# Performance work log

Measured on AMD Instinct MI355X. Metric: run time of the kernel, lower is better.

## Reference

```python
import jax, jax.numpy as jnp
import numpy as np
from jax import lax

B, N, H, D = 4, 384, 8, 5          # graphs, nodes/graph, heads, max multi-hop dist
NE, E_TOT, DH, L = 2048, 8192, 256, 10  # edges/graph, total real edges, d_hidden, curve samples
N_SPATIAL, N_EDGE_DIST = 64, 128


def _bn(x, g, b):
    # eval-mode BatchNorm1d (running_mean=0, running_var=1): affine only
    return x * g + b


def _conv1d(x, w):
    # x: [E, C, L], w: [O, I, 3], SAME padding, stride 1
    return lax.conv_general_dilated(x, w, (1,), 'SAME',
                                    dimension_numbers=('NCH', 'OIH', 'NCH'))


def setup_inputs() -> dict:
    key = jax.random.key(0)
    ks = iter(jax.random.split(key, 64))
    nrm = lambda shape, s=0.02: jax.random.normal(next(ks), shape, jnp.float32) * s
    std = 0.02 / np.sqrt(12.0)  # init_params with n_layer=12 for Linear weights
    inp = {}
    inp['attn_bias'] = jax.random.normal(next(ks), (B, N + 1, N + 1), jnp.float32)
    inp['spatial_pos'] = jax.random.randint(next(ks), (B, N, N), 0, N_SPATIAL)
    inp['d2_dist'] = jax.random.normal(next(ks), (B, N, N, 32), jnp.float32)
    inp['a3_dist'] = jax.random.normal(next(ks), (B, N, N, 32), jnp.float32)
    inp['edge_data'] = jax.random.normal(next(ks), (E_TOT, L, 7), jnp.float32)
    inp['edge_path'] = jax.random.randint(next(ks), (B, N, N, D), 0, NE + 1)
    inp['edge_padding_mask'] = jnp.zeros((B, NE), bool)  # all real edges
    inp['src'] = jax.random.randint(next(ks), (E_TOT,), 0, B * N)
    inp['dst'] = jax.random.randint(next(ks), (E_TOT,), 0, B * N)
    inp['node_data'] = jax.random.normal(next(ks), (B * N, DH), jnp.float32)
    # --- parameters ---
    inp['spatial_emb'] = nrm((N_SPATIAL, H)).at[0].set(0.0)  # padding_idx=0
    inp['t_virtual'] = nrm((1, H))
    inp['w_d2'] = nrm((H, 32), std); inp['b_d2'] = jnp.zeros((H,), jnp.float32)
    inp['w_a3'] = nrm((H, 32), std); inp['b_a3'] = jnp.zeros((H,), jnp.float32)
    inp['cw1'] = nrm((64, 7, 3), std);  inp['cg1'] = jnp.ones((64,));  inp['cb1'] = jnp.zeros((64,))
    inp['cw2'] = nrm((128, 64, 3), std); inp['cg2'] = jnp.ones((128,)); inp['cb2'] = jnp.zeros((128,))
    inp['cw3'] = nrm((256, 128, 3), std); inp['cg3'] = jnp.ones((256,)); inp['cb3'] = jnp.zeros((256,))
    inp['cw_out'] = nrm((H, 256), std)
    # _EdgeConv (UV-Net style): proj Linear(d_hidden->H), MLP(H->64->H), BN, GIN eps
    inp['wp'] = nrm((H, DH), std); inp['bp'] = jnp.zeros((H,))
    inp['w1'] = nrm((64, H), std); inp['b1'] = jnp.zeros((64,))
    inp['g1'] = jnp.ones((64,)); inp['bb1'] = jnp.zeros((64,))
    inp['w2'] = nrm((H, 64), std); inp['b2'] = jnp.zeros((H,))
    inp['g_out'] = jnp.ones((H,)); inp['bb_out'] = jnp.zeros((H,))
    inp['eps'] = jnp.zeros((), jnp.float32)
    inp['edge_dis_w'] = nrm((N_EDGE_DIST * H * H, 1))
    return inp


def reference(attn_bias, spatial_pos, d2_dist, a3_dist, edge_data, edge_path,
              edge_padding_mask, src, dst, node_data, spatial_emb, t_virtual,
              w_d2, b_d2, w_a3, b_a3, cw1, cg1, cb1, cw2, cg2, cb2, cw3, cg3, cb3,
              cw_out, wp, bp, w1, b1, g1, bb1, w2, b2, g_out, bb_out, eps, edge_dis_w):
    gab = jnp.repeat(attn_bias[:, None], H, axis=1)            # [B,H,N+1,N+1]
    spb = spatial_emb[spatial_pos]                              # [B,N,N,H]
    d2b = d2_dist @ w_d2.T + b_d2                               # [B,N,N,H]
    a3b = a3_dist @ w_a3.T + b_a3                               # [B,N,N,H]
    # CurveEncoder on per-edge curve samples
    x = jnp.transpose(edge_data, (0, 2, 1))                     # [E,7,L]
    x = jax.nn.leaky_relu(_bn(_conv1d(x, cw1), cg1[:, None], cb1[:, None]))
    x = jax.nn.leaky_relu(_bn(_conv1d(x, cw2), cg2[:, None], cb2[:, None]))
    x = jax.nn.leaky_relu(_bn(_conv1d(x, cw3), cg3[:, None], cb3[:, None]))
    ef = jnp.mean(x, axis=-1) @ cw_out.T                        # [E,H]
    # _EdgeConv: combine endpoint node features with edge features
    proj = node_data @ wp.T + bp                                # [B*N,H]
    h = (1.0 + eps) * ef + proj[src] + proj[dst]
    h = jax.nn.relu(_bn(h @ w1.T + b1, g1, bb1)) @ w2.T + b2
    edge_out = jax.nn.relu(_bn(h, g_out, bb_out))               # [E,H]
    # scatter real-edge features into padded table (row NE stays zero = padding)
    valid = (~edge_padding_mask).reshape(-1)                    # [B*NE]
    gidx = jnp.maximum(jnp.cumsum(valid) - 1, 0)
    vals = jnp.where(valid[:, None], edge_out[gidx], 0.0).reshape(B, NE, H)
    edge_feature = jnp.zeros((B, NE + 1, H), edge_out.dtype).at[:, :NE].set(vals)
    # gather along multi-hop paths, per-distance head mixing (bmm), normalize
    ep = edge_path.reshape(B, N * N * D)
    edge_input = jax.vmap(lambda f, p: f[p])(edge_feature, ep)  # [B,N*N*D,H]
    edge_input = edge_input.reshape(B, N, N, D, H)
    wdis = edge_dis_w.reshape(-1, H, H)[:D]                     # [D,H,H]
    edge_input = jnp.einsum('bijdh,dhk->bijdk', edge_input, wdis)
    sp = jnp.where(spatial_pos == 0, 1, spatial_pos)
    sp = jnp.where(sp > 1, sp - 1, sp)
    sp = jnp.clip(sp, 0, D)
    edge_bias = edge_input.sum(-2) / sp[..., None].astype(edge_input.dtype)
    inner = spb + d2b + a3b + edge_bias                         # [B,N,N,H]
    gab = gab.at[:, :, 1:, 1:].add(jnp.transpose(inner, (0, 3, 1, 2)))
    t = t_virtual.reshape(1, H, 1)
    gab = gab.at[:, :, 1:, 0].add(t)
    gab = gab.at[:, :, 0, :].add(t)
    return gab + attn_bias[:, None]
```

## Files before the change

kernel.cpp:

```cpp
#include <hip/hip_runtime.h>

#define NB    4
#define NNODE 384
#define NH    8
#define ND    5
#define NEDGE 2048
#define NEP1  2049
#define ETOT  8192
#define DHID  256
#define NP1   385
#define SQ1   (NP1*NP1)
#define NPOS  98304
#define NPOS2 (NPOS + 2)
#define NCELL (NB*NNODE*NNODE)

typedef __attribute__((ext_vector_type(8)))  short short8;
typedef __attribute__((ext_vector_type(16))) float float16;

__device__ __forceinline__ unsigned short f2bf(float f) {
    union { float f; unsigned int u; } v; v.f = f;
    unsigned int u = v.u;
    return (unsigned short)((u + 0x7FFFu + ((u >> 16) & 1u)) >> 16);
}
__device__ __forceinline__ float bf2f(unsigned short s) {
    union { unsigned int u; float f; } v; v.u = ((unsigned int)s) << 16; return v.f;
}
__device__ __forceinline__ unsigned pkbf(float a, float b) {
    return (unsigned)f2bf(a) | ((unsigned)f2bf(b) << 16);
}
__device__ __forceinline__ short8 mk8(unsigned a, unsigned b, unsigned c, unsigned d) {
    union { unsigned u[4]; short8 s; } x; x.u[0]=a; x.u[1]=b; x.u[2]=c; x.u[3]=d; return x.s;
}
__device__ __forceinline__ float leaky(float v) { return v > 0.f ? v : 0.01f * v; }
__device__ __forceinline__ float16 zero16() {
    float16 z;
#pragma unroll
    for (int i = 0; i < 16; ++i) z[i] = 0.f;
    return z;
}
__device__ __forceinline__ void gl_lds16(const void* g, void* l) {
    __builtin_amdgcn_global_load_lds(
        (const __attribute__((address_space(1))) unsigned int*)g,
        (__attribute__((address_space(3))) unsigned int*)l,
        16, 0, 0);
}

__global__ __launch_bounds__(256) void prep_kernel(
    const float* __restrict__ cw1, const float* __restrict__ cw2, const float* __restrict__ cw3,
    const float* __restrict__ cw_out,
    const float* __restrict__ node_data, const float* __restrict__ wp, const float* __restrict__ bp,
    unsigned short* __restrict__ W1f, unsigned short* __restrict__ W2f, unsigned short* __restrict__ W3f,
    unsigned short* __restrict__ Wof,
    float* __restrict__ proj, float* __restrict__ edge_feature)
{
    int gid = blockIdx.x * 256 + threadIdx.x;
    if (gid < 98304) {
        int j = gid & 7, lane = (gid >> 3) & 63, blk = gid >> 9;
        int ks = blk & 7, tp = (blk >> 3) % 3, mt = blk / 24;
        int oc = mt * 32 + (lane & 31);
        int ic = ks * 16 + (lane >> 5) * 8 + j;
        W3f[gid] = f2bf(cw3[(oc * 128 + ic) * 3 + tp]);
    } else if (gid < 122880) {
        int f = gid - 98304;
        int j = f & 7, lane = (f >> 3) & 63, blk = f >> 9;
        int ks = blk & 3, tp = (blk >> 2) % 3, mt = blk / 12;
        int oc = mt * 32 + (lane & 31);
        int ic = ks * 16 + (lane >> 5) * 8 + j;
        W2f[f] = f2bf(cw2[(oc * 64 + ic) * 3 + tp]);
    } else if (gid < 124928) {
        int f = gid - 122880;
        int j = f & 7, lane = (f >> 3) & 63, blk = f >> 9;
        int ks = blk & 1, mt = blk >> 1;
        int oc = mt * 32 + (lane & 31);
        int k = ks * 16 + (lane >> 5) * 8 + j;
        int tp = k >> 3, c = k & 7;
        float v = (tp < 3 && c < 7) ? cw1[oc * 21 + c * 3 + tp] : 0.f;
        W1f[f] = f2bf(v);
    } else if (gid < 137216) {
        int f = gid - 124928;
        int v = f >> 3, h = f & 7;
        const float4* nd4 = (const float4*)(node_data + (size_t)v * DHID);
        const float4* ww4 = (const float4*)(wp + (size_t)h * DHID);
        float s0 = 0.f, s1 = 0.f, s2 = 0.f, s3 = 0.f;
#pragma unroll 4
        for (int c = 0; c < 64; c += 4) {
            float4 x0 = nd4[c+0], y0 = ww4[c+0];
            float4 x1 = nd4[c+1], y1 = ww4[c+1];
            float4 x2 = nd4[c+2], y2 = ww4[c+2];
            float4 x3 = nd4[c+3], y3 = ww4[c+3];
            s0 += x0.x*y0.x + x0.y*y0.y + x0.z*y0.z + x0.w*y0.w;
            s1 += x1.x*y1.x + x1.y*y1.y + x1.z*y1.z + x1.w*y1.w;
            s2 += x2.x*y2.x + x2.y*y2.y + x2.z*y2.z + x2.w*y2.w;
            s3 += x3.x*y3.x + x3.y*y3.y + x3.z*y3.z + x3.w*y3.w;
        }
        proj[f] = bp[h] + (s0 + s1) + (s2 + s3);
    } else if (gid < 137248) {
        int f = gid - 137216;
        int b = f >> 3, h = f & 7;
        edge_feature[((size_t)b * NEP1 + NEDGE) * NH + h] = 0.f;
    } else if (gid < 145440) {
        int f = gid - 137248;
        int j = f & 7, lane = (f >> 3) & 63, g = f >> 9;
        int m = lane & 31;
        int k = g * 16 + (lane >> 5) * 8 + j;
        Wof[f] = (m < 8) ? f2bf(cw_out[m * 256 + k]) : (unsigned short)0;
    }
}

#define X0_GROWS 8
__global__ __launch_bounds__(256) void pack_kernel(
    const float* __restrict__ edge_data,
    unsigned short* __restrict__ X0buf, unsigned short* __restrict__ X1buf,
    unsigned short* __restrict__ X2buf)
{
    int gid = blockIdx.x * 256 + threadIdx.x;
    const int NX0 = (NPOS + 2 * X0_GROWS) * 8;
    if (gid < NX0) {
        int row = gid >> 3, ch = gid & 7;
        int pos = row - X0_GROWS;
        unsigned short v = 0;
        if (pos >= 0 && pos < NPOS && ch < 7) {
            int pm = pos % 12;
            if (pm >= 1 && pm <= 10)
                v = f2bf(edge_data[(size_t)(pos / 12) * 70 + (pm - 1) * 7 + ch]);
        }
        X0buf[gid] = v;
    } else if (gid < NX0 + 128) {
        int f = gid - NX0;
        int p = f >> 5, rest = f & 31;
        int row = (rest >> 4) ? (NPOS + 1) : 0, col = rest & 15;
        X1buf[((size_t)p * NPOS2 + row) * 16 + col] = 0;
    } else if (gid < NX0 + 128 + 256) {
        int f = gid - NX0 - 128;
        int p = f >> 5, rest = f & 31;
        int row = (rest >> 4) ? (NPOS + 1) : 0, col = rest & 15;
        X2buf[((size_t)p * NPOS2 + row) * 16 + col] = 0;
    }
}

__global__ __launch_bounds__(256, 4) void conv1_kernel(
    const unsigned short* __restrict__ X0, const unsigned short* __restrict__ W1f,
    const float* __restrict__ cg1, const float* __restrict__ cb1,
    unsigned short* __restrict__ X1)
{
    const int t = threadIdx.x, wv = t >> 6, lane = t & 63;
    const int q = lane >> 5, n = lane & 31;
    const int pos = blockIdx.x * 128 + wv * 32 + n;

    float16 acc0 = zero16(), acc1 = zero16();
#pragma unroll
    for (int ks = 0; ks < 2; ++ks) {
        short8 b  = *(const short8*)(X0 + (pos - 1 + 2 * ks + q) * 8);
        short8 a0 = *(const short8*)(W1f + ((0 * 2 + ks) * 64 + lane) * 8);
        short8 a1 = *(const short8*)(W1f + ((1 * 2 + ks) * 64 + lane) * 8);
        acc0 = __builtin_amdgcn_mfma_f32_32x32x16_bf16(a0, b, acc0, 0, 0, 0);
        acc1 = __builtin_amdgcn_mfma_f32_32x32x16_bf16(a1, b, acc1, 0, 0, 0);
    }
    int pm = pos % 12;
    bool valid = (pm != 0) && (pm != 11);
#pragma unroll
    for (int mt = 0; mt < 2; ++mt) {
        const float16& acc = mt ? acc1 : acc0;
#pragma unroll
        for (int r2 = 0; r2 < 4; ++r2) {
            int oc0 = mt * 32 + 8 * r2 + 4 * q;
            float4 g4 = *(const float4*)(cg1 + oc0);
            float4 b4 = *(const float4*)(cb1 + oc0);
            unsigned short uu[4];
            uu[0] = valid ? f2bf(leaky(acc[r2*4+0] * g4.x + b4.x)) : (unsigned short)0;
            uu[1] = valid ? f2bf(leaky(acc[r2*4+1] * g4.y + b4.y)) : (unsigned short)0;
            uu[2] = valid ? f2bf(leaky(acc[r2*4+2] * g4.z + b4.z)) : (unsigned short)0;
            uu[3] = valid ? f2bf(leaky(acc[r2*4+3] * g4.w + b4.w)) : (unsigned short)0;
            uint2 pk; pk.x = uu[0] | ((unsigned)uu[1] << 16); pk.y = uu[2] | ((unsigned)uu[3] << 16);
            *(uint2*)(void*)(X1 + ((size_t)(oc0 >> 4) * NPOS2 + pos + 1) * 16 + (oc0 & 15)) = pk;
        }
    }
}

__global__ __launch_bounds__(256, 4) void conv2_kernel(
    const unsigned short* __restrict__ X1, const unsigned short* __restrict__ W2f,
    const float* __restrict__ cg2, const float* __restrict__ cb2,
    unsigned short* __restrict__ X2)
{
    __shared__ __align__(16) unsigned short sB[4][1568];
    const int t = threadIdx.x, wv = t >> 6, lane = t & 63;
    const int q = lane >> 5, n = lane & 31;
    const int base = blockIdx.x * 96;
    const int cbase = (wv < 3) ? wv * 64 : 132;

#pragma unroll
    for (int ks = 0; ks < 4; ++ks)
        gl_lds16(X1 + ((size_t)ks * NPOS2 + base) * 16 + (cbase + lane) * 8,
                 &sB[ks][cbase * 8]);

    float16 acc[3];
#pragma unroll
    for (int nt = 0; nt < 3; ++nt) acc[nt] = zero16();

    __syncthreads();

#pragma unroll
    for (int ks = 0; ks < 4; ++ks)
#pragma unroll
        for (int tp = 0; tp < 3; ++tp) {
            short8 a = *(const short8*)(W2f + (((wv * 3 + tp) * 4 + ks) * 64 + lane) * 8);
#pragma unroll
            for (int nt = 0; nt < 3; ++nt) {
                short8 b = *(const short8*)(&sB[ks][(nt * 32 + n + tp) * 16 + q * 8]);
                acc[nt] = __builtin_amdgcn_mfma_f32_32x32x16_bf16(a, b, acc[nt], 0, 0, 0);
            }
        }

#pragma unroll
    for (int nt = 0; nt < 3; ++nt) {
        int pos = base + nt * 32 + n;
        int pm = pos % 12;
        bool valid = (pm != 0) && (pm != 11);
#pragma unroll
        for (int r2 = 0; r2 < 4; ++r2) {
            int oc0 = wv * 32 + 8 * r2 + 4 * q;
            float4 g4 = *(const float4*)(cg2 + oc0);
            float4 b4 = *(const float4*)(cb2 + oc0);
            unsigned short uu[4];
            uu[0] = valid ? f2bf(leaky(acc[nt][r2*4+0] * g4.x + b4.x)) : (unsigned short)0;
            uu[1] = valid ? f2bf(leaky(acc[nt][r2*4+1] * g4.y + b4.y)) : (unsigned short)0;
            uu[2] = valid ? f2bf(leaky(acc[nt][r2*4+2] * g4.z + b4.z)) : (unsigned short)0;
            uu[3] = valid ? f2bf(leaky(acc[nt][r2*4+3] * g4.w + b4.w)) : (unsigned short)0;
            uint2 pk; pk.x = uu[0] | ((unsigned)uu[1] << 16); pk.y = uu[2] | ((unsigned)uu[3] << 16);
            *(uint2*)(void*)(X2 + ((size_t)(oc0 >> 4) * NPOS2 + pos + 1) * 16 + (oc0 & 15)) = pk;
        }
    }
}

__global__ __launch_bounds__(256, 3) void conv3_kernel(
    const unsigned short* __restrict__ X2, const unsigned short* __restrict__ W3f,
    const unsigned short* __restrict__ Wof,
    const float* __restrict__ cg3, const float* __restrict__ cb3,
    const int* __restrict__ src, const int* __restrict__ dst,
    const float* __restrict__ w1, const float* __restrict__ b1,
    const float* __restrict__ g1, const float* __restrict__ bb1,
    const float* __restrict__ w2, const float* __restrict__ b2,
    const float* __restrict__ g_out, const float* __restrict__ bb_out,
    const float* __restrict__ eps, const float* __restrict__ proj,
    float* __restrict__ edge_feature)
{
    __shared__ __align__(16) unsigned char smem3[25088];
    unsigned short* sB = (unsigned short*)smem3;
    float* fs = (float*)smem3;
    const int t = threadIdx.x, wv = t >> 6, lane = t & 63;
    const int q = lane >> 5, n = lane & 31;
    const int base = blockIdx.x * 96;
    const int cbase = (wv < 3) ? wv * 64 : 132;

#pragma unroll
    for (int ks = 0; ks < 8; ++ks)
        gl_lds16(X2 + ((size_t)ks * NPOS2 + base) * 16 + (cbase + lane) * 8,
                 &sB[ks * 1568 + cbase * 8]);

    float16 acc[2][3];
#pragma unroll
    for (int i = 0; i < 2; ++i)
#pragma unroll
        for (int nt = 0; nt < 3; ++nt) acc[i][nt] = zero16();

    __syncthreads();

#pragma unroll
    for (int ks = 0; ks < 8; ++ks)
#pragma unroll
        for (int tp = 0; tp < 3; ++tp) {
            short8 a0 = *(const short8*)(W3f + ((((wv*2+0) * 3 + tp) * 8 + ks) * 64 + lane) * 8);
            short8 a1 = *(const short8*)(W3f + ((((wv*2+1) * 3 + tp) * 8 + ks) * 64 + lane) * 8);
#pragma unroll
            for (int nt = 0; nt < 3; ++nt) {
                short8 b = *(const short8*)(&sB[ks * 1568 + (nt * 32 + n + tp) * 16 + q * 8]);
                acc[0][nt] = __builtin_amdgcn_mfma_f32_32x32x16_bf16(a0, b, acc[0][nt], 0, 0, 0);
                acc[1][nt] = __builtin_amdgcn_mfma_f32_32x32x16_bf16(a1, b, acc[1][nt], 0, 0, 0);
            }
        }

    __syncthreads();

    short8 wof[4];
#pragma unroll
    for (int g = 0; g < 4; ++g)
        wof[g] = *(const short8*)(Wof + ((wv * 4 + g) * 64 + lane) * 8);

#pragma unroll
    for (int nt = 0; nt < 3; ++nt) {
        int pm = (nt * 32 + n) % 12;
        bool valid = (pm != 0) && (pm != 11);
        float16 p = zero16();
#pragma unroll
        for (int i = 0; i < 2; ++i) {
            int mt = wv * 2 + i;
            float av[16];
#pragma unroll
            for (int r2 = 0; r2 < 4; ++r2) {
                int oc0 = mt * 32 + 8 * r2 + 4 * q;
                float4 g4 = *(const float4*)(cg3 + oc0);
                float4 b4 = *(const float4*)(cb3 + oc0);
                av[r2*4+0] = valid ? leaky(acc[i][nt][r2*4+0] * g4.x + b4.x) : 0.f;
                av[r2*4+1] = valid ? leaky(acc[i][nt][r2*4+1] * g4.y + b4.y) : 0.f;
                av[r2*4+2] = valid ? leaky(acc[i][nt][r2*4+2] * g4.z + b4.z) : 0.f;
                av[r2*4+3] = valid ? leaky(acc[i][nt][r2*4+3] * g4.w + b4.w) : 0.f;
            }
            unsigned pk[8], op[8];
#pragma unroll
            for (int z = 0; z < 8; ++z) pk[z] = pkbf(av[2*z], av[2*z+1]);
#pragma unroll
            for (int z = 0; z < 8; ++z) op[z] = __shfl_xor((int)pk[z], 32);
            short8 f0 = q == 0 ? mk8(pk[0], pk[1], op[0], op[1])
                               : mk8(op[2], op[3], pk[2], pk[3]);
            short8 f1 = q == 0 ? mk8(pk[4], pk[5], op[4], op[5])
                               : mk8(op[6], op[7], pk[6], pk[7]);
            p = __builtin_amdgcn_mfma_f32_32x32x16_bf16(wof[i*2+0], f0, p, 0, 0, 0);
            p = __builtin_amdgcn_mfma_f32_32x32x16_bf16(wof[i*2+1], f1, p, 0, 0, 0);
        }
        float4 st = make_float4(p[0], p[1], p[2], p[3]);
        *(float4*)&fs[((wv * 96) + nt * 32 + n) * 8 + 4 * q] = st;
    }
    __syncthreads();

    if (t < 64) {
        int e = t >> 3, h = t & 7;
        float s = 0.f;
#pragma unroll
        for (int w = 0; w < 4; ++w)
#pragma unroll 4
            for (int l = 0; l < 12; ++l) s += fs[(w * 96 + e * 12 + l) * 8 + h];
        float efv = 0.1f * s;
        int ge = blockIdx.x * 8 + e;
        fs[3072 + e * 8 + h] = (1.f + eps[0]) * efv
                             + proj[src[ge] * NH + h] + proj[dst[ge] * NH + h];
    }
    __syncthreads();

#pragma unroll
    for (int bb = 0; bb < 512; bb += 256) {
        int idx = bb + t;
        int e = idx >> 6, o = idx & 63;
        float a = b1[o];
#pragma unroll
        for (int h = 0; h < 8; ++h) a += fs[3072 + e * 8 + h] * w1[o * 8 + h];
        float v = a * g1[o] + bb1[o];
        fs[3136 + e * 64 + o] = v > 0.f ? v : 0.f;
    }
    __syncthreads();

    if (t < 64) {
        int e = t >> 3, h = t & 7;
        float a = b2[h];
#pragma unroll 8
        for (int o = 0; o < 64; ++o) a += fs[3136 + e * 64 + o] * w2[h * 64 + o];
        float v = a * g_out[h] + bb_out[h];
        v = v > 0.f ? v : 0.f;
        int ge = blockIdx.x * 8 + e;
        int b = ge >> 11, el2 = ge & (NEDGE - 1);
        edge_feature[((size_t)b * NEP1 + el2) * NH + h] = v;
    }
}

__global__ __launch_bounds__(256) void eins_kernel(
    const float* __restrict__ d2_dist, const float* __restrict__ a3_dist,
    const float* __restrict__ w_d2, const float* __restrict__ w_a3,
    unsigned short* __restrict__ acc8)
{
    const int t = threadIdx.x, part = t & 7;
    float4 wd[8], wa[8];
#pragma unroll
    for (int h = 0; h < 8; ++h) {
        wd[h] = *(const float4*)(w_d2 + h * 32 + part * 4);
        wa[h] = *(const float4*)(w_a3 + h * 32 + part * 4);
    }
    const bool pb0 = part & 1, pb1 = (part >> 1) & 1, pb2 = (part >> 2) & 1;
    const size_t stride = 73728;
    size_t cell = (size_t)blockIdx.x * 32 + (t >> 3);

    float4 vd = ((const float4*)(d2_dist + cell * 32))[part];
    float4 va = ((const float4*)(a3_dist + cell * 32))[part];
#pragma unroll 1
    for (int it = 0; it < 8; ++it) {
        float4 nvd = vd, nva = va;
        if (it < 7) {
            nvd = ((const float4*)(d2_dist + (cell + stride) * 32))[part];
            nva = ((const float4*)(a3_dist + (cell + stride) * 32))[part];
        }
        float acc[8];
#pragma unroll
        for (int h = 0; h < 8; ++h)
            acc[h] = vd.x*wd[h].x + vd.y*wd[h].y + vd.z*wd[h].z + vd.w*wd[h].w
                   + va.x*wa[h].x + va.y*wa[h].y + va.z*wa[h].z + va.w*wa[h].w;
        float y0 = (pb0 ? acc[1] : acc[0]) + __shfl_xor(pb0 ? acc[0] : acc[1], 1, 64);
        float y1 = (pb0 ? acc[3] : acc[2]) + __shfl_xor(pb0 ? acc[2] : acc[3], 1, 64);
        float y2 = (pb0 ? acc[5] : acc[4]) + __shfl_xor(pb0 ? acc[4] : acc[5], 1, 64);
        float y3 = (pb0 ? acc[7] : acc[6]) + __shfl_xor(pb0 ? acc[6] : acc[7], 1, 64);
        float z0 = (pb1 ? y1 : y0) + __shfl_xor(pb1 ? y0 : y1, 2, 64);
        float z1 = (pb1 ? y3 : y2) + __shfl_xor(pb1 ? y2 : y3, 2, 64);
        float rr = (pb2 ? z1 : z0) + __shfl_xor(pb2 ? z0 : z1, 4, 64);
        acc8[cell * 8 + part] = f2bf(rr);
        cell += stride;
        vd = nvd; va = nva;
    }
}

__global__ __launch_bounds__(256) void tbl_kernel(
    const float* __restrict__ edge_feature, const float* __restrict__ edge_dis_w,
    float* __restrict__ T)
{
    int idx = blockIdx.x * 256 + threadIdx.x;
    if (idx >= NEP1 * 8) return;
    int pi = idx >> 3, k = idx & 7;
    int d = blockIdx.y, b = blockIdx.z;
    const float* ef = edge_feature + ((size_t)b * NEP1 + pi) * NH;
    const float* w  = edge_dis_w + d * 64 + k;
    float s = 0.f;
#pragma unroll
    for (int h = 0; h < 8; ++h) s += ef[h] * w[h * 8];
    T[(((size_t)b * ND + d) * NEP1 + pi) * 8 + k] = s;
}

__global__ __launch_bounds__(256) void bias_kernel(
    const float* __restrict__ attn_bias, const int* __restrict__ spatial_pos,
    const int* __restrict__ edge_path,
    const float* __restrict__ spatial_emb, const float* __restrict__ t_virtual,
    const float* __restrict__ b_d2, const float* __restrict__ b_a3,
    const float* __restrict__ Tbl, const unsigned short* __restrict__ acc8,
    float* __restrict__ out)
{
    __shared__ __align__(16) float s_emb[512];
    int t = threadIdx.x;
    for (int i = t; i < 512; i += 256) s_emb[i] = spatial_emb[i];
    __syncthreads();

    int gc = blockIdx.x * 256 + t;
    if (gc >= NB * SQ1) return;
    int b = gc / SQ1, rem = gc % SQ1;
    int i = rem / NP1, j = rem % NP1;
    float base = 2.f * attn_bias[gc];
    bool border = (i == 0) || (j == 0);

    float res[8];
    if (border) {
#pragma unroll
        for (int h = 0; h < 8; ++h) res[h] = base + t_virtual[h];
    } else {
        size_t nidx = ((size_t)b * NNODE + (i - 1)) * NNODE + (j - 1);
        int sp = spatial_pos[nidx];
        union { uint4 u; unsigned short s[8]; } aa;
        aa.u = *(const uint4*)(acc8 + nidx * 8);
        const int* ep = edge_path + nidx * ND;
        const float* Tb = Tbl + (size_t)b * (ND * NEP1 * 8);
        float edp[8] = {0,0,0,0,0,0,0,0};
#pragma unroll
        for (int d = 0; d < ND; ++d) {
            const float* r = Tb + ((size_t)d * NEP1 + ep[d]) * 8;
            float4 r0 = *(const float4*)r;
            float4 r1 = *(const float4*)(r + 4);
            edp[0] += r0.x; edp[1] += r0.y; edp[2] += r0.z; edp[3] += r0.w;
            edp[4] += r1.x; edp[5] += r1.y; edp[6] += r1.z; edp[7] += r1.w;
        }
        int spd = (sp == 0) ? 1 : sp;
        spd = (spd > 1) ? spd - 1 : spd;
        spd = (spd > ND) ? ND : spd;
        float inv = 1.f / (float)spd;
        const float* em = s_emb + sp * 8;
#pragma unroll
        for (int h = 0; h < 8; ++h)
            res[h] = base + bf2f(aa.s[h]) + edp[h] * inv + em[h] + b_d2[h] + b_a3[h];
    }
#pragma unroll
    for (int h = 0; h < 8; ++h)
        out[((size_t)b * NH + h) * SQ1 + rem] = res[h];
}

extern "C" void kernel_launch(void* const* d_in, const int* in_sizes, int n_in,
                              void* d_out, int out_size, void* d_ws, size_t ws_size,
                              hipStream_t stream)
{
    const float* attn_bias   = (const float*)d_in[0];
    const int*   spatial_pos = (const int*)  d_in[1];
    const float* d2_dist     = (const float*)d_in[2];
    const float* a3_dist     = (const float*)d_in[3];
    const float* edge_data   = (const float*)d_in[4];
    const int*   edge_path   = (const int*)  d_in[5];
    const int*   src         = (const int*)  d_in[7];
    const int*   dst         = (const int*)  d_in[8];
    const float* node_data   = (const float*)d_in[9];
    const float* spatial_emb = (const float*)d_in[10];
    const float* t_virtual   = (const float*)d_in[11];
    const float* w_d2        = (const float*)d_in[12];
    const float* b_d2        = (const float*)d_in[13];
    const float* w_a3        = (const float*)d_in[14];
    const float* b_a3        = (const float*)d_in[15];
    const float* cw1         = (const float*)d_in[16];
    const float* cg1         = (const float*)d_in[17];
    const float* cb1         = (const float*)d_in[18];
    const float* cw2         = (const float*)d_in[19];
    const float* cg2         = (const float*)d_in[20];
    const float* cb2         = (const float*)d_in[21];
    const float* cw3         = (const float*)d_in[22];
    const float* cg3         = (const float*)d_in[23];
    const float* cb3         = (const float*)d_in[24];
    const float* cw_out      = (const float*)d_in[25];
    const float* wp          = (const float*)d_in[26];
    const float* bp          = (const float*)d_in[27];
    const float* w1          = (const float*)d_in[28];
    const float* b1          = (const float*)d_in[29];
    const float* g1          = (const float*)d_in[30];
    const float* bb1         = (const float*)d_in[31];
    const float* w2          = (const float*)d_in[32];
    const float* b2          = (const float*)d_in[33];
    const float* g_out       = (const float*)d_in[34];
    const float* bb_out      = (const float*)d_in[35];
    const float* eps         = (const float*)d_in[36];
    const float* edge_dis_w  = (const float*)d_in[37];

    float*          proj  = (float*)d_ws;
    float*          ef    = proj + NB * NNODE * NH;
    unsigned short* W1f   = (unsigned short*)(ef + NB * NEP1 * NH);
    unsigned short* W2f   = W1f + 2048;
    unsigned short* W3f   = W2f + 24576;
    unsigned short* Wof   = W3f + 98304;
    unsigned short* X0buf = Wof + 8192;
    unsigned short* X1buf = X0buf + (size_t)(NPOS + 2 * X0_GROWS) * 8;
    unsigned short* X2buf = X1buf + (size_t)4 * NPOS2 * 16;
    unsigned short* X0 = X0buf + X0_GROWS * 8;
    float*          Tbl   = (float*)X0buf;
    unsigned short* acc8  = X1buf;

    prep_kernel<<<569, 256, 0, stream>>>(cw1, cw2, cw3, cw_out, node_data, wp, bp,
                                         W1f, W2f, W3f, Wof, proj, ef);
    pack_kernel<<<3074, 256, 0, stream>>>(edge_data, X0buf, X1buf, X2buf);

    conv1_kernel<<<NPOS / 128, 256, 0, stream>>>(X0, W1f, cg1, cb1, X1buf);
    conv2_kernel<<<NPOS / 96, 256, 0, stream>>>(X1buf, W2f, cg2, cb2, X2buf);

    eins_kernel<<<2304, 256, 0, stream>>>(d2_dist, a3_dist, w_d2, w_a3, acc8);

    conv3_kernel<<<NPOS / 96, 256, 0, stream>>>(X2buf, W3f, Wof, cg3, cb3,
                                                src, dst, w1, b1, g1, bb1,
                                                w2, b2, g_out, bb_out, eps,
                                                proj, ef);

    dim3 tgrid((NEP1 * 8 + 255) / 256, ND, NB);
    tbl_kernel<<<tgrid, 256, 0, stream>>>(ef, edge_dis_w, Tbl);

    int nbias = (NB * SQ1 + 255) / 256;
    bias_kernel<<<nbias, 256, 0, stream>>>(
        attn_bias, spatial_pos, edge_path,
        spatial_emb, t_virtual, b_d2, b_a3,
        Tbl, acc8, (float*)d_out);
}
```

Baseline: 358.7 us.

## Make conv kernels persistent with register-resident weights and double-buffered LDS tiles

conv2 and conv3 now hold their weight fragments and BN scale/shift in registers. Each block loops over several 96-position tiles, prefetching the next tile into a second LDS buffer while the current one is computed. conv3 splits its output channels across a second grid dimension, writes partial projections to a global buffer, and hands the edge MLP to a new edge_tail_kernel. The intent is to cut repeated weight loads and hide global-to-LDS latency, at the cost of more registers, lower occupancy, an extra kernel launch and a global round trip. The eins kernel is moved after conv3 and tbl because Pglob aliases the buffer it writes.

```diff
diff --git a/kernel.cpp b/kernel.cpp
--- a/kernel.cpp
+++ b/kernel.cpp
@@ -177,65 +177,185 @@
     }
 }
 
-__global__ __launch_bounds__(256, 4) void conv2_kernel(
+__global__ __launch_bounds__(256, 2) void conv2_kernel(
     const unsigned short* __restrict__ X1, const unsigned short* __restrict__ W2f,
     const float* __restrict__ cg2, const float* __restrict__ cb2,
     unsigned short* __restrict__ X2)
 {
-    __shared__ __align__(16) unsigned short sB[4][1568];
+    __shared__ __align__(16) unsigned short sB[2][4 * 1568];
     const int t = threadIdx.x, wv = t >> 6, lane = t & 63;
     const int q = lane >> 5, n = lane & 31;
-    const int base = blockIdx.x * 96;
     const int cbase = (wv < 3) ? wv * 64 : 132;
+    const int pbase0 = blockIdx.x * 192;
+
+    short8 a[3][4];
+#pragma unroll
+    for (int tp = 0; tp < 3; ++tp)
+#pragma unroll
+        for (int ks = 0; ks < 4; ++ks)
+            a[tp][ks] = *(const short8*)(W2f + (((wv * 3 + tp) * 4 + ks) * 64 + lane) * 8);
+
+    float4 g4[4], b4[4];
+#pragma unroll
+    for (int r2 = 0; r2 < 4; ++r2) {
+        g4[r2] = *(const float4*)(cg2 + wv * 32 + 8 * r2 + 4 * q);
+        b4[r2] = *(const float4*)(cb2 + wv * 32 + 8 * r2 + 4 * q);
+    }
 
 #pragma unroll
     for (int ks = 0; ks < 4; ++ks)
-        gl_lds16(X1 + ((size_t)ks * NPOS2 + base) * 16 + (cbase + lane) * 8,
-                 &sB[ks][cbase * 8]);
-
-    float16 acc[3];
-#pragma unroll
-    for (int nt = 0; nt < 3; ++nt) acc[nt] = zero16();
-
-    __syncthreads();
-
-#pragma unroll
-    for (int ks = 0; ks < 4; ++ks)
-#pragma unroll
-        for (int tp = 0; tp < 3; ++tp) {
-            short8 a = *(const short8*)(W2f + (((wv * 3 + tp) * 4 + ks) * 64 + lane) * 8);
-#pragma unroll
-            for (int nt = 0; nt < 3; ++nt) {
-                short8 b = *(const short8*)(&sB[ks][(nt * 32 + n + tp) * 16 + q * 8]);
-                acc[nt] = __builtin_amdgcn_mfma_f32_32x32x16_bf16(a, b, acc[nt], 0, 0, 0);
+        gl_lds16(X1 + ((size_t)ks * NPOS2 + pbase0) * 16 + (cbase + lane) * 8,
+                 &sB[0][ks * 1568 + cbase * 8]);
+
+#pragma unroll 1
+    for (int pt = 0; pt < 2; ++pt) {
+        const int cur = pt & 1;
+        const int base = pbase0 + pt * 96;
+        __syncthreads();
+        if (pt < 1) {
+#pragma unroll
+            for (int ks = 0; ks < 4; ++ks)
+                gl_lds16(X1 + ((size_t)ks * NPOS2 + base + 96) * 16 + (cbase + lane) * 8,
+                         &sB[cur ^ 1][ks * 1568 + cbase * 8]);
+        }
+        float16 acc[3];
+#pragma unroll
+        for (int nt = 0; nt < 3; ++nt) acc[nt] = zero16();
+#pragma unroll
+        for (int ks = 0; ks < 4; ++ks)
+#pragma unroll
+            for (int tp = 0; tp < 3; ++tp)
+#pragma unroll
+                for (int nt = 0; nt < 3; ++nt) {
+                    short8 b = *(const short8*)(&sB[cur][ks * 1568 + (nt * 32 + n + tp) * 16 + q * 8]);
+                    acc[nt] = __builtin_amdgcn_mfma_f32_32x32x16_bf16(a[tp][ks], b, acc[nt], 0, 0, 0);
+                }
+#pragma unroll
+        for (int nt = 0; nt < 3; ++nt) {
+            int pos = base + nt * 32 + n;
+            int pm = (nt * 32 + n) % 12;
+            bool valid = (pm != 0) && (pm != 11);
+#pragma unroll
+            for (int r2 = 0; r2 < 4; ++r2) {
+                int oc0 = wv * 32 + 8 * r2 + 4 * q;
+                unsigned short uu[4];
+                uu[0] = valid ? f2bf(leaky(acc[nt][r2*4+0] * g4[r2].x + b4[r2].x)) : (unsigned short)0;
+                uu[1] = valid ? f2bf(leaky(acc[nt][r2*4+1] * g4[r2].y + b4[r2].y)) : (unsigned short)0;
+                uu[2] = valid ? f2bf(leaky(acc[nt][r2*4+2] * g4[r2].z + b4[r2].z)) : (unsigned short)0;
+                uu[3] = valid ? f2bf(leaky(acc[nt][r2*4+3] * g4[r2].w + b4[r2].w)) : (unsigned short)0;
+                uint2 pk; pk.x = uu[0] | ((unsigned)uu[1] << 16); pk.y = uu[2] | ((unsigned)uu[3] << 16);
+                *(uint2*)(void*)(X2 + ((size_t)(oc0 >> 4) * NPOS2 + pos + 1) * 16 + (oc0 & 15)) = pk;
             }
         }
-
-#pragma unroll
-    for (int nt = 0; nt < 3; ++nt) {
-        int pos = base + nt * 32 + n;
-        int pm = pos % 12;
-        bool valid = (pm != 0) && (pm != 11);
-#pragma unroll
-        for (int r2 = 0; r2 < 4; ++r2) {
-            int oc0 = wv * 32 + 8 * r2 + 4 * q;
-            float4 g4 = *(const float4*)(cg2 + oc0);
-            float4 b4 = *(const float4*)(cb2 + oc0);
-            unsigned short uu[4];
-            uu[0] = valid ? f2bf(leaky(acc[nt][r2*4+0] * g4.x + b4.x)) : (unsigned short)0;
-            uu[1] = valid ? f2bf(leaky(acc[nt][r2*4+1] * g4.y + b4.y)) : (unsigned short)0;
-            uu[2] = valid ? f2bf(leaky(acc[nt][r2*4+2] * g4.z + b4.z)) : (unsigned short)0;
-            uu[3] = valid ? f2bf(leaky(acc[nt][r2*4+3] * g4.w + b4.w)) : (unsigned short)0;
-            uint2 pk; pk.x = uu[0] | ((unsigned)uu[1] << 16); pk.y = uu[2] | ((unsigned)uu[3] << 16);
-            *(uint2*)(void*)(X2 + ((size_t)(oc0 >> 4) * NPOS2 + pos + 1) * 16 + (oc0 & 15)) = pk;
-        }
-    }
-}
-
-__global__ __launch_bounds__(256, 3) void conv3_kernel(
+    }
+}
+
+__global__ __launch_bounds__(256, 2) void conv3_kernel(
     const unsigned short* __restrict__ X2, const unsigned short* __restrict__ W3f,
     const unsigned short* __restrict__ Wof,
     const float* __restrict__ cg3, const float* __restrict__ cb3,
+    float* __restrict__ Pglob)
+{
+    __shared__ __align__(16) unsigned short sB[2][8 * 1568];
+    __shared__ float fs[768];
+    const int t = threadIdx.x, wv = t >> 6, lane = t & 63;
+    const int q = lane >> 5, n = lane & 31;
+    const int gy = blockIdx.y;
+    const int mt = gy * 4 + wv;
+    const int cbase = (wv < 3) ? wv * 64 : 132;
+    const int pbase0 = blockIdx.x * 384;
+
+    short8 a[3][8];
+#pragma unroll
+    for (int tp = 0; tp < 3; ++tp)
+#pragma unroll
+        for (int ks = 0; ks < 8; ++ks)
+            a[tp][ks] = *(const short8*)(W3f + (((mt * 3 + tp) * 8 + ks) * 64 + lane) * 8);
+    short8 wof0 = *(const short8*)(Wof + ((2 * mt + 0) * 64 + lane) * 8);
+    short8 wof1 = *(const short8*)(Wof + ((2 * mt + 1) * 64 + lane) * 8);
+
+    float4 g4[4], b4[4];
+#pragma unroll
+    for (int r2 = 0; r2 < 4; ++r2) {
+        g4[r2] = *(const float4*)(cg3 + mt * 32 + 8 * r2 + 4 * q);
+        b4[r2] = *(const float4*)(cb3 + mt * 32 + 8 * r2 + 4 * q);
+    }
+
+#pragma unroll
+    for (int ks = 0; ks < 8; ++ks)
+        gl_lds16(X2 + ((size_t)ks * NPOS2 + pbase0) * 16 + (cbase + lane) * 8,
+                 &sB[0][ks * 1568 + cbase * 8]);
+
+#pragma unroll 1
+    for (int pt = 0; pt < 4; ++pt) {
+        const int cur = pt & 1;
+        const int base = pbase0 + pt * 96;
+        __syncthreads();
+        if (pt < 3) {
+#pragma unroll
+            for (int ks = 0; ks < 8; ++ks)
+                gl_lds16(X2 + ((size_t)ks * NPOS2 + base + 96) * 16 + (cbase + lane) * 8,
+                         &sB[cur ^ 1][ks * 1568 + cbase * 8]);
+        }
+        fs[t] = 0.f; fs[256 + t] = 0.f; fs[512 + t] = 0.f;
+
+        float16 acc[3];
+#pragma unroll
+        for (int nt = 0; nt < 3; ++nt) acc[nt] = zero16();
+#pragma unroll
+        for (int ks = 0; ks < 8; ++ks)
+#pragma unroll
+            for (int tp = 0; tp < 3; ++tp)
+#pragma unroll
+                for (int nt = 0; nt < 3; ++nt) {
+                    short8 b = *(const short8*)(&sB[cur][ks * 1568 + (nt * 32 + n + tp) * 16 + q * 8]);
+                    acc[nt] = __builtin_amdgcn_mfma_f32_32x32x16_bf16(a[tp][ks], b, acc[nt], 0, 0, 0);
+                }
+
+        float4 pout[3];
+#pragma unroll
+        for (int nt = 0; nt < 3; ++nt) {
+            int pm = (nt * 32 + n) % 12;
+            bool valid = (pm != 0) && (pm != 11);
+            float av[16];
+#pragma unroll
+            for (int r2 = 0; r2 < 4; ++r2) {
+                av[r2*4+0] = valid ? leaky(acc[nt][r2*4+0] * g4[r2].x + b4[r2].x) : 0.f;
+                av[r2*4+1] = valid ? leaky(acc[nt][r2*4+1] * g4[r2].y + b4[r2].y) : 0.f;
+                av[r2*4+2] = valid ? leaky(acc[nt][r2*4+2] * g4[r2].z + b4[r2].z) : 0.f;
+                av[r2*4+3] = valid ? leaky(acc[nt][r2*4+3] * g4[r2].w + b4[r2].w) : 0.f;
+            }
+            unsigned pk[8], op[8];
+#pragma unroll
+            for (int z = 0; z < 8; ++z) pk[z] = pkbf(av[2*z], av[2*z+1]);
+#pragma unroll
+            for (int z = 0; z < 8; ++z) op[z] = __shfl_xor((int)pk[z], 32);
+            short8 f0 = q == 0 ? mk8(pk[0], pk[1], op[0], op[1])
+                               : mk8(op[2], op[3], pk[2], pk[3]);
+            short8 f1 = q == 0 ? mk8(pk[4], pk[5], op[4], op[5])
+                               : mk8(op[6], op[7], pk[6], pk[7]);
+            float16 p = zero16();
+            p = __builtin_amdgcn_mfma_f32_32x32x16_bf16(wof0, f0, p, 0, 0, 0);
+            p = __builtin_amdgcn_mfma_f32_32x32x16_bf16(wof1, f1, p, 0, 0, 0);
+            pout[nt] = make_float4(p[0], p[1], p[2], p[3]);
+        }
+        __syncthreads();
+#pragma unroll
+        for (int nt = 0; nt < 3; ++nt) {
+            int o = (nt * 32 + n) * 8 + 4 * q;
+            atomicAdd(&fs[o + 0], pout[nt].x);
+            atomicAdd(&fs[o + 1], pout[nt].y);
+            atomicAdd(&fs[o + 2], pout[nt].z);
+            atomicAdd(&fs[o + 3], pout[nt].w);
+        }
+        __syncthreads();
+        float* Pg = Pglob + ((size_t)gy * NPOS + base) * 8;
+        Pg[t] = fs[t]; Pg[256 + t] = fs[256 + t]; Pg[512 + t] = fs[512 + t];
+    }
+}
+
+__global__ __launch_bounds__(256) void edge_tail_kernel(
+    const float* __restrict__ Pglob,
     const int* __restrict__ src, const int* __restrict__ dst,
     const float* __restrict__ w1, const float* __restrict__ b1,
     const float* __restrict__ g1, const float* __restrict__ bb1,
@@ -244,121 +364,41 @@
     const float* __restrict__ eps, const float* __restrict__ proj,
     float* __restrict__ edge_feature)
 {
-    __shared__ __align__(16) unsigned char smem3[25088];
-    unsigned short* sB = (unsigned short*)smem3;
-    float* fs = (float*)smem3;
-    const int t = threadIdx.x, wv = t >> 6, lane = t & 63;
-    const int q = lane >> 5, n = lane & 31;
-    const int base = blockIdx.x * 96;
-    const int cbase = (wv < 3) ? wv * 64 : 132;
-
-#pragma unroll
-    for (int ks = 0; ks < 8; ++ks)
-        gl_lds16(X2 + ((size_t)ks * NPOS2 + base) * 16 + (cbase + lane) * 8,
-                 &sB[ks * 1568 + cbase * 8]);
-
-    float16 acc[2][3];
-#pragma unroll
-    for (int i = 0; i < 2; ++i)
-#pragma unroll
-        for (int nt = 0; nt < 3; ++nt) acc[i][nt] = zero16();
-
+    __shared__ float s_h[32 * 8];
+    __shared__ float s_t1[32 * 64];
+    const int t = threadIdx.x;
+    const int e = t >> 3, h = t & 7;
+    const int ge = blockIdx.x * 32 + e;
+
+    const float* P0 = Pglob + (size_t)(ge * 12) * 8 + h;
+    const float* P1 = Pglob + ((size_t)NPOS + ge * 12) * 8 + h;
+    float s = 0.f;
+#pragma unroll
+    for (int l = 0; l < 12; ++l) s += P0[l * 8] + P1[l * 8];
+    float efv = 0.1f * s;
+    s_h[e * 8 + h] = (1.f + eps[0]) * efv
+                   + proj[src[ge] * NH + h] + proj[dst[ge] * NH + h];
     __syncthreads();
 
 #pragma unroll
-    for (int ks = 0; ks < 8; ++ks)
-#pragma unroll
-        for (int tp = 0; tp < 3; ++tp) {
-            short8 a0 = *(const short8*)(W3f + ((((wv*2+0) * 3 + tp) * 8 + ks) * 64 + lane) * 8);
-            short8 a1 = *(const short8*)(W3f + ((((wv*2+1) * 3 + tp) * 8 + ks) * 64 + lane) * 8);
-#pragma unroll
-            for (int nt = 0; nt < 3; ++nt) {
-                short8 b = *(const short8*)(&sB[ks * 1568 + (nt * 32 + n + tp) * 16 + q * 8]);
-                acc[0][nt] = __builtin_amdgcn_mfma_f32_32x32x16_bf16(a0, b, acc[0][nt], 0, 0, 0);
-                acc[1][nt] = __builtin_amdgcn_mfma_f32_32x32x16_bf16(a1, b, acc[1][nt], 0, 0, 0);
-            }
-        }
-
+    for (int r = 0; r < 8; ++r) {
+        int idx = r * 256 + t;
+        int ee = idx >> 6, o = idx & 63;
+        float a = b1[o];
+#pragma unroll
+        for (int h2 = 0; h2 < 8; ++h2) a += s_h[ee * 8 + h2] * w1[o * 8 + h2];
+        float v = a * g1[o] + bb1[o];
+        s_t1[ee * 64 + o] = v > 0.f ? v : 0.f;
+    }
     __syncthreads();
 
-    short8 wof[4];
-#pragma unroll
-    for (int g = 0; g < 4; ++g)
-        wof[g] = *(const short8*)(Wof + ((wv * 4 + g) * 64 + lane) * 8);
-
-#pragma unroll
-    for (int nt = 0; nt < 3; ++nt) {
-        int pm = (nt * 32 + n) % 12;
-        bool valid = (pm != 0) && (pm != 11);
-        float16 p = zero16();
-#pragma unroll
-        for (int i = 0; i < 2; ++i) {
-            int mt = wv * 2 + i;
-            float av[16];
-#pragma unroll
-            for (int r2 = 0; r2 < 4; ++r2) {
-                int oc0 = mt * 32 + 8 * r2 + 4 * q;
-                float4 g4 = *(const float4*)(cg3 + oc0);
-                float4 b4 = *(const float4*)(cb3 + oc0);
-                av[r2*4+0] = valid ? leaky(acc[i][nt][r2*4+0] * g4.x + b4.x) : 0.f;
-                av[r2*4+1] = valid ? leaky(acc[i][nt][r2*4+1] * g4.y + b4.y) : 0.f;
-                av[r2*4+2] = valid ? leaky(acc[i][nt][r2*4+2] * g4.z + b4.z) : 0.f;
-                av[r2*4+3] = valid ? leaky(acc[i][nt][r2*4+3] * g4.w + b4.w) : 0.f;
-            }
-            unsigned pk[8], op[8];
-#pragma unroll
-            for (int z = 0; z < 8; ++z) pk[z] = pkbf(av[2*z], av[2*z+1]);
-#pragma unroll
-            for (int z = 0; z < 8; ++z) op[z] = __shfl_xor((int)pk[z], 32);
-            short8 f0 = q == 0 ? mk8(pk[0], pk[1], op[0], op[1])
-                               : mk8(op[2], op[3], pk[2], pk[3]);
-            short8 f1 = q == 0 ? mk8(pk[4], pk[5], op[4], op[5])
-                               : mk8(op[6], op[7], pk[6], pk[7]);
-            p = __builtin_amdgcn_mfma_f32_32x32x16_bf16(wof[i*2+0], f0, p, 0, 0, 0);
-            p = __builtin_amdgcn_mfma_f32_32x32x16_bf16(wof[i*2+1], f1, p, 0, 0, 0);
-        }
-        float4 st = make_float4(p[0], p[1], p[2], p[3]);
-        *(float4*)&fs[((wv * 96) + nt * 32 + n) * 8 + 4 * q] = st;
-    }
-    __syncthreads();
-
-    if (t < 64) {
-        int e = t >> 3, h = t & 7;
-        float s = 0.f;
-#pragma unroll
-        for (int w = 0; w < 4; ++w)
-#pragma unroll 4
-            for (int l = 0; l < 12; ++l) s += fs[(w * 96 + e * 12 + l) * 8 + h];
-        float efv = 0.1f * s;
-        int ge = blockIdx.x * 8 + e;
-        fs[3072 + e * 8 + h] = (1.f + eps[0]) * efv
-                             + proj[src[ge] * NH + h] + proj[dst[ge] * NH + h];
-    }
-    __syncthreads();
-
-#pragma unroll
-    for (int bb = 0; bb < 512; bb += 256) {
-        int idx = bb + t;
-        int e = idx >> 6, o = idx & 63;
-        float a = b1[o];
-#pragma unroll
-        for (int h = 0; h < 8; ++h) a += fs[3072 + e * 8 + h] * w1[o * 8 + h];
-        float v = a * g1[o] + bb1[o];
-        fs[3136 + e * 64 + o] = v > 0.f ? v : 0.f;
-    }
-    __syncthreads();
-
-    if (t < 64) {
-        int e = t >> 3, h = t & 7;
-        float a = b2[h];
+    float a = b2[h];
 #pragma unroll 8
-        for (int o = 0; o < 64; ++o) a += fs[3136 + e * 64 + o] * w2[h * 64 + o];
-        float v = a * g_out[h] + bb_out[h];
-        v = v > 0.f ? v : 0.f;
-        int ge = blockIdx.x * 8 + e;
-        int b = ge >> 11, el2 = ge & (NEDGE - 1);
-        edge_feature[((size_t)b * NEP1 + el2) * NH + h] = v;
-    }
+    for (int o = 0; o < 64; ++o) a += s_t1[e * 64 + o] * w2[h * 64 + o];
+    float v = a * g_out[h] + bb_out[h];
+    v = v > 0.f ? v : 0.f;
+    int b = ge >> 11, el = ge & (NEDGE - 1);
+    edge_feature[((size_t)b * NEP1 + el) * NH + h] = v;
 }
 
 __global__ __launch_bounds__(256) void eins_kernel(
@@ -527,6 +567,7 @@
     unsigned short* X2buf = X1buf + (size_t)4 * NPOS2 * 16;
     unsigned short* X0 = X0buf + X0_GROWS * 8;
     float*          Tbl   = (float*)X0buf;
+    float*          Pglob = (float*)X1buf;
     unsigned short* acc8  = X1buf;
 
     prep_kernel<<<569, 256, 0, stream>>>(cw1, cw2, cw3, cw_out, node_data, wp, bp,
@@ -534,17 +575,19 @@
     pack_kernel<<<3074, 256, 0, stream>>>(edge_data, X0buf, X1buf, X2buf);
 
     conv1_kernel<<<NPOS / 128, 256, 0, stream>>>(X0, W1f, cg1, cb1, X1buf);
-    conv2_kernel<<<NPOS / 96, 256, 0, stream>>>(X1buf, W2f, cg2, cb2, X2buf);
-
-    eins_kernel<<<2304, 256, 0, stream>>>(d2_dist, a3_dist, w_d2, w_a3, acc8);
-
-    conv3_kernel<<<NPOS / 96, 256, 0, stream>>>(X2buf, W3f, Wof, cg3, cb3,
-                                                src, dst, w1, b1, g1, bb1,
-                                                w2, b2, g_out, bb_out, eps,
-                                                proj, ef);
+    conv2_kernel<<<NPOS / 192, 256, 0, stream>>>(X1buf, W2f, cg2, cb2, X2buf);
+
+    dim3 c3grid(NPOS / 384, 2);
+    conv3_kernel<<<c3grid, 256, 0, stream>>>(X2buf, W3f, Wof, cg3, cb3, Pglob);
+
+    edge_tail_kernel<<<ETOT / 32, 256, 0, stream>>>(Pglob, src, dst,
+                                                    w1, b1, g1, bb1, w2, b2,
+                                                    g_out, bb_out, eps, proj, ef);
 
     dim3 tgrid((NEP1 * 8 + 255) / 256, ND, NB);
     tbl_kernel<<<tgrid, 256, 0, stream>>>(ef, edge_dis_w, Tbl);
+
+    eins_kernel<<<2304, 256, 0, stream>>>(d2_dist, a3_dist, w_d2, w_a3, acc8);
 
     int nbias = (NB * SQ1 + 255) / 256;
     bias_kernel<<<nbias, 256, 0, stream>>>(
```

Result: slower. 389.7 us (+8.6%).
